# Performance work log

Measured on AMD Instinct MI355X. Metric: run time of the kernel, lower is better.

The kernel has to match this reference:

```python
import jax, jax.numpy as jnp
import numpy as np

PAD, BOS, EOS = 0, 1, 2
VOCAB, EMB, HID, N, T = 32, 32, 512, 4096, 64


def _lstm_step(x, h, c, W_ih, W_hh, b_ih, b_hh):
    # PyTorch nn.LSTM single step; gate order [i|f|g|o]
    g = x @ W_ih.T + h @ W_hh.T + b_ih + b_hh  # [n, 4H]
    i, f, gg, o = jnp.split(g, 4, axis=-1)
    i = jax.nn.sigmoid(i)
    f = jax.nn.sigmoid(f)
    gg = jnp.tanh(gg)
    o = jax.nn.sigmoid(o)
    c = f * c + i * gg
    h = o * jnp.tanh(c)
    return h, c


def setup_inputs() -> dict:
    key = jax.random.key(0)
    ks = jax.random.split(key, 12)
    s = 0.04  # ~1/sqrt(hidden), matches torch LSTM init scale
    emb = jax.random.normal(ks[0], (VOCAB, EMB), jnp.float32) * s
    emb = emb.at[PAD].set(0.0)  # padding_idx row is zero
    inp = {
        "prevs": jnp.full((N, 1), BOS, dtype=jnp.int32),
        "emb": emb,
        "W_ih0": jax.random.normal(ks[1], (4 * HID, EMB), jnp.float32) * s,
        "W_hh0": jax.random.normal(ks[2], (4 * HID, HID), jnp.float32) * s,
        "b_ih0": jax.random.normal(ks[3], (4 * HID,), jnp.float32) * s,
        "b_hh0": jax.random.normal(ks[4], (4 * HID,), jnp.float32) * s,
        "W_ih1": jax.random.normal(ks[5], (4 * HID, HID), jnp.float32) * s,
        "W_hh1": jax.random.normal(ks[6], (4 * HID, HID), jnp.float32) * s,
        "b_ih1": jax.random.normal(ks[7], (4 * HID,), jnp.float32) * s,
        "b_hh1": jax.random.normal(ks[8], (4 * HID,), jnp.float32) * s,
        "W_out": jax.random.normal(ks[9], (VOCAB, HID), jnp.float32) * s,
        "b_out": jax.random.normal(ks[10], (VOCAB,), jnp.float32) * s,
        "max_length": T,
    }
    return inp


def reference(prevs, emb, W_ih0, W_hh0, b_ih0, b_hh0,
              W_ih1, W_hh1, b_ih1, b_hh1, W_out, b_out, max_length):
    # softmax+multinomial sampling, <eos>/<pad> bookkeeping.
    n = prevs.shape[0]
    H = W_hh0.shape[1]
    keys = jax.random.split(jax.random.key(7), max_length)
    tok0 = prevs[:, 0]
    h0 = jnp.zeros((n, H), emb.dtype)
    init = (tok0, h0, h0, h0, h0,
            tok0 == EOS, jnp.zeros((n,), jnp.int32))

    def step(carry, key):
        tok, h0, c0, h1, c1, is_end, lengths = carry
        x = emb[tok]                                   # [n, EMB]
        h0, c0 = _lstm_step(x, h0, c0, W_ih0, W_hh0, b_ih0, b_hh0)
        h1, c1 = _lstm_step(h0, h1, c1, W_ih1, W_hh1, b_ih1, b_hh1)
        logits = h1 @ W_out.T + b_out                  # [n, VOCAB]
        sampled = jax.random.categorical(key, logits)  # == multinomial(softmax)
        cur = jnp.where(is_end, PAD, sampled).astype(tok.dtype)
        lengths = lengths + (~is_end).astype(jnp.int32)
        is_end = is_end | (cur == EOS)
        return (cur, h0, c0, h1, c1, is_end, lengths), cur

    carry, toks = jax.lax.scan(step, init, keys)       # toks: [T, n]
    lengths = carry[-1] + 1                            # +1 for <bos>
    samples = jnp.concatenate([prevs, toks.T], axis=1)  # [n, 1+T]
    return samples, lengths
```

## Files before the change

### kernel.cpp

```cpp
#include <hip/hip_runtime.h>
#include <cstdint>
#include <cmath>

#define RNG_VARIANT 1

#define NROWS 4096
#define HIDN 512
#define VOC 32
#define TSTEPS 64
#define PAD_TOK 0
#define BOS_TOK 1
#define EOS_TOK 2

#define BK 32
#define BM 128
#define JJT 32

typedef const __attribute__((address_space(1))) unsigned int* gptr_t;
typedef __attribute__((address_space(3))) unsigned int* lptr_t;

__host__ __device__ inline void tf2x32(unsigned k0, unsigned k1, unsigned x0, unsigned x1,
                                       unsigned& o0, unsigned& o1) {
  unsigned ks0 = k0, ks1 = k1, ks2 = k0 ^ k1 ^ 0x1BD11BDAu;
  unsigned X0 = x0 + ks0, X1 = x1 + ks1;
  const unsigned R[5][4] = {{13,15,26,6},{17,29,16,24},{13,15,26,6},{17,29,16,24},{13,15,26,6}};
  unsigned inj0[5], inj1[5];
  inj0[0] = ks1; inj1[0] = ks2;
  inj0[1] = ks2; inj1[1] = ks0;
  inj0[2] = ks0; inj1[2] = ks1;
  inj0[3] = ks1; inj1[3] = ks2;
  inj0[4] = ks2; inj1[4] = ks0;
#pragma unroll
  for (int i = 0; i < 5; ++i) {
#pragma unroll
    for (int j = 0; j < 4; ++j) {
      X0 += X1;
      unsigned r = R[i][j];
      X1 = (X1 << r) | (X1 >> (32 - r));
      X1 ^= X0;
    }
    X0 += inj0[i];
    X1 += inj1[i] + (unsigned)(i + 1);
  }
  o0 = X0; o1 = X1;
}

template<int NPARTS, bool LAYER0>
__global__ __launch_bounds__(256, 2) void lstm_fused(
    const float* __restrict__ A0, const float* __restrict__ B0,
    const float* __restrict__ A1, const float* __restrict__ B1,
    const float* __restrict__ extra,
    const int* __restrict__ tokv,
    const int* __restrict__ list, const int* __restrict__ cnt, int t,
    float* __restrict__ h, float* __restrict__ c)
{
  const int nact = cnt[t];
  const int m0 = blockIdx.y * BM;
  if (m0 >= nact) return;

  __shared__ float As[2][BM * BK];
  __shared__ float Bs[2][BM * BK];
  const int tid = threadIdx.x;
  const int lane = tid & 63;
  const int w = tid >> 6;
  const int wr = w >> 1, wc = w & 1;
  const int ty = lane >> 3, tx = lane & 7;
  const int c0 = blockIdx.x * JJT;
  const int toff = t * NROWS;

  const int g8 = lane >> 3;
  const int ch = lane & 7;

  int ra[4];
#pragma unroll
  for (int i = 0; i < 4; ++i) {
    const int slot = m0 + w * 32 + i * 8 + g8;
    ra[i] = (slot < nact) ? list[toff + slot] : 0;
  }

  float acc[8][8];
#pragma unroll
  for (int i = 0; i < 8; ++i)
#pragma unroll
    for (int j = 0; j < 8; ++j) acc[i][j] = 0.f;

  const int NT = NPARTS * (HIDN / BK);

  auto STAGE = [&](int tt, int sel) {
    const float* A = A0;
    const float* B = B0;
    if (NPARTS == 2 && (tt >> 4)) { A = A1; B = B1; }
    const int kb = (tt & 15) * BK;
    float* dA = &As[sel][0];
    float* dB = &Bs[sel][0];
#pragma unroll
    for (int i = 0; i < 4; ++i) {
      const int rbase = w * 32 + i * 8;
      const int swz = (rbase >> 3) & 7;
      const float* sA = A + (size_t)ra[i] * HIDN + kb + ((ch ^ swz) << 2);
      __builtin_amdgcn_global_load_lds((gptr_t)sA, (lptr_t)(dA + rbase * BK), 16, 0, 0);
      const int mB = rbase + g8;
      const int grB = (mB & 3) * HIDN + c0 + (mB >> 2);
      const float* sB = B + (size_t)grB * HIDN + kb + ((ch ^ swz) << 2);
      __builtin_amdgcn_global_load_lds((gptr_t)sB, (lptr_t)(dB + rbase * BK), 16, 0, 0);
    }
  };

  STAGE(0, 0);
  __syncthreads();
  int sel = 0;
  const int aRow = wr * 64 + ty * 8;
  const int bRow = wc * 64 + tx * 8;
  for (int tt = 0; tt < NT; ++tt) {
    if (tt + 1 < NT) STAGE(tt + 1, sel ^ 1);
    const float* As_ = &As[sel][0];
    const float* Bs_ = &Bs[sel][0];
#pragma unroll
    for (int kg = 0; kg < 8; ++kg) {
      float4 av[8], bv[8];
#pragma unroll
      for (int i = 0; i < 8; ++i)
        av[i] = *(const float4*)(As_ + (aRow + i) * BK + ((kg ^ ty) << 2));
#pragma unroll
      for (int j = 0; j < 8; ++j)
        bv[j] = *(const float4*)(Bs_ + (bRow + j) * BK + ((kg ^ tx) << 2));
#pragma unroll
      for (int i = 0; i < 8; ++i)
#pragma unroll
        for (int j = 0; j < 8; ++j)
          acc[i][j] = fmaf(av[i].x, bv[j].x, acc[i][j]);
#pragma unroll
      for (int i = 0; i < 8; ++i)
#pragma unroll
        for (int j = 0; j < 8; ++j)
          acc[i][j] = fmaf(av[i].y, bv[j].y, acc[i][j]);
#pragma unroll
      for (int i = 0; i < 8; ++i)
#pragma unroll
        for (int j = 0; j < 8; ++j)
          acc[i][j] = fmaf(av[i].z, bv[j].z, acc[i][j]);
#pragma unroll
      for (int i = 0; i < 8; ++i)
#pragma unroll
        for (int j = 0; j < 8; ++j)
          acc[i][j] = fmaf(av[i].w, bv[j].w, acc[i][j]);
    }
    __syncthreads();
    sel ^= 1;
  }

  const int jjl = wc * 16 + tx * 2;
  const size_t colb = (size_t)(c0 + jjl);
  float e[8];
  if (!LAYER0) {
    float4 e0 = *(const float4*)(extra + colb * 4);
    float4 e1 = *(const float4*)(extra + colb * 4 + 4);
    e[0] = e0.x; e[1] = e0.y; e[2] = e0.z; e[3] = e0.w;
    e[4] = e1.x; e[5] = e1.y; e[6] = e1.z; e[7] = e1.w;
  }
#pragma unroll
  for (int i = 0; i < 8; ++i) {
    const int slot = m0 + wr * 64 + ty * 8 + i;
    if (slot >= nact) continue;
    const int n = list[toff + slot];
    if (LAYER0) {
      const int tk = tokv[n];
      const float* ex = extra + (size_t)tk * 2048 + colb * 4;
      float4 e0 = *(const float4*)(ex);
      float4 e1 = *(const float4*)(ex + 4);
      e[0] = e0.x; e[1] = e0.y; e[2] = e0.z; e[3] = e0.w;
      e[4] = e1.x; e[5] = e1.y; e[6] = e1.z; e[7] = e1.w;
    }
    float gi0 = acc[i][0] + e[0], gf0 = acc[i][1] + e[1];
    float gg0 = acc[i][2] + e[2], go0 = acc[i][3] + e[3];
    float gi1 = acc[i][4] + e[4], gf1 = acc[i][5] + e[5];
    float gg1 = acc[i][6] + e[6], go1 = acc[i][7] + e[7];
    const size_t idx = (size_t)n * HIDN + colb;
    float2 cold = *(const float2*)(c + idx);
    float si0 = 1.f / (1.f + expf(-gi0));
    float sf0 = 1.f / (1.f + expf(-gf0));
    float tg0 = tanhf(gg0);
    float so0 = 1.f / (1.f + expf(-go0));
    float cn0 = sf0 * cold.x + si0 * tg0;
    float hn0 = so0 * tanhf(cn0);
    float si1 = 1.f / (1.f + expf(-gi1));
    float sf1 = 1.f / (1.f + expf(-gf1));
    float tg1 = tanhf(gg1);
    float so1 = 1.f / (1.f + expf(-go1));
    float cn1 = sf1 * cold.y + si1 * tg1;
    float hn1 = so1 * tanhf(cn1);
    *(float2*)(c + idx) = make_float2(cn0, cn1);
    *(float2*)(h + idx) = make_float2(hn0, hn1);
  }
}

__global__ void build_ew0(const float* __restrict__ emb, const float* __restrict__ W_ih0,
                          const float* __restrict__ b_ih0, const float* __restrict__ b_hh0,
                          float* __restrict__ EW0i)
{
  int idx = blockIdx.x * 256 + threadIdx.x;
  int vv = idx >> 11, j = idx & 2047;
  float s = b_ih0[j] + b_hh0[j];
#pragma unroll
  for (int e = 0; e < 32; ++e)
    s = fmaf(emb[vv * 32 + e], W_ih0[(size_t)j * 32 + e], s);
  EW0i[(size_t)vv * 2048 + (size_t)(j & 511) * 4 + (j >> 9)] = s;
}

__global__ void build_bias1i(const float* __restrict__ a, const float* __restrict__ b,
                             float* __restrict__ o) {
  int j = blockIdx.x * 256 + threadIdx.x;
  o[(size_t)(j & 511) * 4 + (j >> 9)] = a[j] + b[j];
}

__global__ void init_state(const int* __restrict__ prevs, int* __restrict__ tok,
                           int* __restrict__ lengths, int* __restrict__ out,
                           int* __restrict__ list, int* __restrict__ cnt)
{
  int n = blockIdx.x * 256 + threadIdx.x;
  if (n < NROWS) {
    int p = prevs[n];
    tok[n] = p;
    lengths[n] = 0;
    out[(size_t)n * (TSTEPS + 1)] = p;
    if (p != EOS_TOK) {
      int pos = atomicAdd(&cnt[0], 1);
      list[pos] = n;
    }
  }
}

__global__ __launch_bounds__(64) void sample_step(
    const float* __restrict__ h1, const float* __restrict__ W_out,
    const float* __restrict__ b_out,
    int* __restrict__ tok, int* __restrict__ lengths,
    int* __restrict__ out, int* __restrict__ list, int* __restrict__ cnt,
    unsigned key0, unsigned key1, int t)
{
  const int nact = cnt[t];
  const int b = blockIdx.x;
  if (b >= nact) return;
  const int n = list[t * NROWS + b];

  __shared__ float hrow[HIDN];
  const int lane = threadIdx.x;
  {
    const float4* src = reinterpret_cast<const float4*>(h1 + (size_t)n * HIDN);
    float4* dst = reinterpret_cast<float4*>(hrow);
    dst[lane] = src[lane];
    dst[lane + 64] = src[lane + 64];
  }
  __syncthreads();
  const int v = lane & 31, half = lane >> 5;
  const float* wp = W_out + (size_t)v * HIDN + half * 256;
  const float* hh = hrow + half * 256;
  float dot = 0.f;
#pragma unroll
  for (int k = 0; k < 256; k += 4) {
    float4 wv = *reinterpret_cast<const float4*>(wp + k);
    float4 hv = *reinterpret_cast<const float4*>(hh + k);
    dot = fmaf(wv.x, hv.x, dot);
    dot = fmaf(wv.y, hv.y, dot);
    dot = fmaf(wv.z, hv.z, dot);
    dot = fmaf(wv.w, hv.w, dot);
  }
  dot += __shfl_xor(dot, 32);
  const float logit = dot + b_out[v];

  const unsigned iflat = (unsigned)(n * 32 + v);
  unsigned r0, r1, bits;
#if RNG_VARIANT == 1
  tf2x32(key0, key1, 0u, iflat, r0, r1);
  bits = r0 ^ r1;
#elif RNG_VARIANT == 2
  if (iflat < 65536u) { tf2x32(key0, key1, iflat, iflat + 65536u, r0, r1); bits = r0; }
  else                { tf2x32(key0, key1, iflat - 65536u, iflat, r0, r1); bits = r1; }
#else
  tf2x32(key0, key1, 0u, iflat, r0, r1);
  bits = r1;
#endif
  float f = __uint_as_float((bits >> 9) | 0x3f800000u) - 1.0f;
  float u = fmaxf(f, 1.1754943508222875e-38f);
  float t1 = -(float)log((double)u);
  float g  = -(float)log((double)t1);
  float s = g + logit;

  float bs = s; int bi = v;
#pragma unroll
  for (int off = 16; off >= 1; off >>= 1) {
    float os = __shfl_xor(bs, off);
    int   oi = __shfl_xor(bi, off);
    if (os > bs || (os == bs && oi < bi)) { bs = os; bi = oi; }
  }
  if (lane == 0) {
    const int cur = bi;
    lengths[n] = lengths[n] + 1;
    tok[n] = cur;
    out[(size_t)n * (TSTEPS + 1) + t + 1] = cur;
    if (cur != EOS_TOK) {
      int pos = atomicAdd(&cnt[t + 1], 1);
      list[(t + 1) * NROWS + pos] = n;
    }
  }
}

__global__ void final_lengths(const int* __restrict__ lengths, int* __restrict__ out)
{
  int n = blockIdx.x * 256 + threadIdx.x;
  if (n < NROWS) out[(size_t)NROWS * (TSTEPS + 1) + n] = lengths[n] + 1;
}

extern "C" void kernel_launch(void* const* d_in, const int* in_sizes, int n_in,
                              void* d_out, int out_size, void* d_ws, size_t ws_size,
                              hipStream_t stream)
{
  const int*   prevs = (const int*)d_in[0];
  const float* emb   = (const float*)d_in[1];
  const float* W_ih0 = (const float*)d_in[2];
  const float* W_hh0 = (const float*)d_in[3];
  const float* b_ih0 = (const float*)d_in[4];
  const float* b_hh0 = (const float*)d_in[5];
  const float* W_ih1 = (const float*)d_in[6];
  const float* W_hh1 = (const float*)d_in[7];
  const float* b_ih1 = (const float*)d_in[8];
  const float* b_hh1 = (const float*)d_in[9];
  const float* W_out = (const float*)d_in[10];
  const float* b_out = (const float*)d_in[11];

  const size_t S = (size_t)NROWS * HIDN;
  float* h0a   = (float*)d_ws;
  float* h1a   = h0a + S;
  float* cl0   = h1a + S;
  float* cl1   = cl0 + S;
  float* h0b   = cl1 + S;
  float* h1b   = h0b + S;
  float* EW0i  = h1b + S;
  float* bias1i = EW0i + (size_t)VOC * 2048;
  int* tok     = (int*)(bias1i + 2048);
  int* lengths = tok + NROWS;
  int* list    = lengths + NROWS;
  int* cnt     = list + (TSTEPS + 1) * NROWS;
  int* outp    = (int*)d_out;

  hipMemsetAsync(h0a, 0, 4 * S * sizeof(float), stream);
  hipMemsetAsync(cnt, 0, (TSTEPS + 1) * sizeof(int), stream);
  hipMemsetAsync(outp, 0, (size_t)out_size * sizeof(int), stream);
  init_state<<<NROWS / 256, 256, 0, stream>>>(prevs, tok, lengths, outp, list, cnt);
  build_ew0<<<VOC * 2048 / 256, 256, 0, stream>>>(emb, W_ih0, b_ih0, b_hh0, EW0i);
  build_bias1i<<<2048 / 256, 256, 0, stream>>>(b_ih1, b_hh1, bias1i);

  unsigned keys[TSTEPS][2];
  for (int t = 0; t < TSTEPS; ++t) {
    unsigned o0, o1;
    tf2x32(0u, 7u, 0u, (unsigned)t, o0, o1);
    keys[t][0] = o0; keys[t][1] = o1;
  }

  dim3 ggrid(HIDN / JJT, NROWS / BM);
  for (int t = 0; t < TSTEPS; ++t) {
    float* h0rd = (t & 1) ? h0b : h0a;
    float* h0wr = (t & 1) ? h0a : h0b;
    float* h1rd = (t & 1) ? h1b : h1a;
    float* h1wr = (t & 1) ? h1a : h1b;
    lstm_fused<1, true><<<ggrid, 256, 0, stream>>>(
        h0rd, W_hh0, nullptr, nullptr, EW0i, tok, list, cnt, t, h0wr, cl0);
    lstm_fused<2, false><<<ggrid, 256, 0, stream>>>(
        h0wr, W_ih1, h1rd, W_hh1, bias1i, nullptr, list, cnt, t, h1wr, cl1);
    sample_step<<<NROWS, 64, 0, stream>>>(h1wr, W_out, b_out, tok, lengths, outp,
                                          list, cnt, keys[t][0], keys[t][1], t);
  }
  final_lengths<<<NROWS / 256, 256, 0, stream>>>(lengths, outp);
}
```

Measured before the change: 21.32 ms.

## Retile fused LSTM GEMM to 128x256 tiles with 512 threads and BK=16

Changes the gate GEMM tile from 128 rows x 128 gate-columns (32 hidden units) to 128 rows x 256 gate-columns (64 hidden units), using 8 waves per block instead of 4 and a K-slice of 16 instead of 32. The staging code is reworked so each thread issues one A and two B direct-to-LDS loads per slice, with a new XOR swizzle for the 16-wide rows. This halves the grid's column dimension, raising reuse of each A tile, and doubles the number of K iterations and barriers per block. The launch-bound hint of 4 blocks of 512 threads per CU may squeeze the 64-float accumulator plus operands into fewer registers, risking spills.

```diff
diff --git a/kernel.cpp b/kernel.cpp
--- a/kernel.cpp
+++ b/kernel.cpp
@@ -12,9 +12,9 @@
 #define BOS_TOK 1
 #define EOS_TOK 2
 
-#define BK 32
+#define BKK 16
 #define BM 128
-#define JJT 32
+#define BNG 64
 
 typedef const __attribute__((address_space(1))) unsigned int* gptr_t;
 typedef __attribute__((address_space(3))) unsigned int* lptr_t;
@@ -46,7 +46,7 @@
 }
 
 template<int NPARTS, bool LAYER0>
-__global__ __launch_bounds__(256, 2) void lstm_fused(
+__global__ __launch_bounds__(512, 4) void lstm_fused(
     const float* __restrict__ A0, const float* __restrict__ B0,
     const float* __restrict__ A1, const float* __restrict__ B1,
     const float* __restrict__ extra,
@@ -58,24 +58,26 @@
   const int m0 = blockIdx.y * BM;
   if (m0 >= nact) return;
 
-  __shared__ float As[2][BM * BK];
-  __shared__ float Bs[2][BM * BK];
+  __shared__ float As[2][BM * BKK];
+  __shared__ float Bs[2][4 * BNG * BKK];
   const int tid = threadIdx.x;
   const int lane = tid & 63;
   const int w = tid >> 6;
-  const int wr = w >> 1, wc = w & 1;
+  const int wr = w >> 2, wc = w & 3;
   const int ty = lane >> 3, tx = lane & 7;
-  const int c0 = blockIdx.x * JJT;
+  const int c0 = blockIdx.x * BNG;
   const int toff = t * NROWS;
 
-  const int g8 = lane >> 3;
-  const int ch = lane & 7;
-
-  int ra[4];
-#pragma unroll
-  for (int i = 0; i < 4; ++i) {
-    const int slot = m0 + w * 32 + i * 8 + g8;
-    ra[i] = (slot < nact) ? list[toff + slot] : 0;
+  const int aslot = m0 + (tid >> 2);
+  const int ra = (aslot < nact) ? list[toff + aslot] : 0;
+
+  const int schunk = (((tid & 3) ^ ((tid >> 5) & 3)) << 2);
+
+  int brow[2];
+#pragma unroll
+  for (int p = 0; p < 2; ++p) {
+    const int jq = p * 128 + (tid >> 2);
+    brow[p] = (jq & 3) * HIDN + c0 + (jq >> 2);
   }
 
   float acc[8][8];
@@ -84,26 +86,19 @@
 #pragma unroll
     for (int j = 0; j < 8; ++j) acc[i][j] = 0.f;
 
-  const int NT = NPARTS * (HIDN / BK);
+  const int NT = NPARTS * (HIDN / BKK);
 
   auto STAGE = [&](int tt, int sel) {
     const float* A = A0;
     const float* B = B0;
-    if (NPARTS == 2 && (tt >> 4)) { A = A1; B = B1; }
-    const int kb = (tt & 15) * BK;
-    float* dA = &As[sel][0];
-    float* dB = &Bs[sel][0];
-#pragma unroll
-    for (int i = 0; i < 4; ++i) {
-      const int rbase = w * 32 + i * 8;
-      const int swz = (rbase >> 3) & 7;
-      const float* sA = A + (size_t)ra[i] * HIDN + kb + ((ch ^ swz) << 2);
-      __builtin_amdgcn_global_load_lds((gptr_t)sA, (lptr_t)(dA + rbase * BK), 16, 0, 0);
-      const int mB = rbase + g8;
-      const int grB = (mB & 3) * HIDN + c0 + (mB >> 2);
-      const float* sB = B + (size_t)grB * HIDN + kb + ((ch ^ swz) << 2);
-      __builtin_amdgcn_global_load_lds((gptr_t)sB, (lptr_t)(dB + rbase * BK), 16, 0, 0);
-    }
+    if (NPARTS == 2 && (tt >> 5)) { A = A1; B = B1; }
+    const int kb = (tt & 31) * BKK;
+    __builtin_amdgcn_global_load_lds((gptr_t)(A + (size_t)ra * HIDN + kb + schunk),
+        (lptr_t)(&As[sel][w * 256]), 16, 0, 0);
+    __builtin_amdgcn_global_load_lds((gptr_t)(B + (size_t)brow[0] * HIDN + kb + schunk),
+        (lptr_t)(&Bs[sel][w * 256]), 16, 0, 0);
+    __builtin_amdgcn_global_load_lds((gptr_t)(B + (size_t)brow[1] * HIDN + kb + schunk),
+        (lptr_t)(&Bs[sel][2048 + w * 256]), 16, 0, 0);
   };
 
   STAGE(0, 0);
@@ -111,19 +106,21 @@
   int sel = 0;
   const int aRow = wr * 64 + ty * 8;
   const int bRow = wc * 64 + tx * 8;
+  const int aCx = ty & 3;
+  const int bCx = tx & 3;
   for (int tt = 0; tt < NT; ++tt) {
     if (tt + 1 < NT) STAGE(tt + 1, sel ^ 1);
     const float* As_ = &As[sel][0];
     const float* Bs_ = &Bs[sel][0];
 #pragma unroll
-    for (int kg = 0; kg < 8; ++kg) {
+    for (int kg = 0; kg < 4; ++kg) {
       float4 av[8], bv[8];
 #pragma unroll
       for (int i = 0; i < 8; ++i)
-        av[i] = *(const float4*)(As_ + (aRow + i) * BK + ((kg ^ ty) << 2));
+        av[i] = *(const float4*)(As_ + (aRow + i) * BKK + ((kg ^ aCx) << 2));
 #pragma unroll
       for (int j = 0; j < 8; ++j)
-        bv[j] = *(const float4*)(Bs_ + (bRow + j) * BK + ((kg ^ tx) << 2));
+        bv[j] = *(const float4*)(Bs_ + (bRow + j) * BKK + ((kg ^ bCx) << 2));
 #pragma unroll
       for (int i = 0; i < 8; ++i)
 #pragma unroll
@@ -160,7 +157,7 @@
   }
 #pragma unroll
   for (int i = 0; i < 8; ++i) {
-    const int slot = m0 + wr * 64 + ty * 8 + i;
+    const int slot = m0 + aRow + i;
     if (slot >= nact) continue;
     const int n = list[toff + slot];
     if (LAYER0) {
@@ -356,15 +353,15 @@
     keys[t][0] = o0; keys[t][1] = o1;
   }
 
-  dim3 ggrid(HIDN / JJT, NROWS / BM);
+  dim3 ggrid(HIDN / BNG, NROWS / BM);
   for (int t = 0; t < TSTEPS; ++t) {
     float* h0rd = (t & 1) ? h0b : h0a;
     float* h0wr = (t & 1) ? h0a : h0b;
     float* h1rd = (t & 1) ? h1b : h1a;
     float* h1wr = (t & 1) ? h1a : h1b;
-    lstm_fused<1, true><<<ggrid, 256, 0, stream>>>(
+    lstm_fused<1, true><<<ggrid, 512, 0, stream>>>(
         h0rd, W_hh0, nullptr, nullptr, EW0i, tok, list, cnt, t, h0wr, cl0);
-    lstm_fused<2, false><<<ggrid, 256, 0, stream>>>(
+    lstm_fused<2, false><<<ggrid, 512, 0, stream>>>(
         h0wr, W_ih1, h1rd, W_hh1, bias1i, nullptr, list, cnt, t, h1wr, cl1);
     sample_step<<<NROWS, 64, 0, stream>>>(h1wr, W_out, b_out, tok, lengths, outp,
                                           list, cnt, keys[t][0], keys[t][1], t);
```

New measurement: 28.56 ms. 1.34x slower.
